# Kernel tuning notes

Hardware: AMD Instinct MI355X
Metric: run time of the kernel (lower is better)

Reference implementation:

```python
import jax, jax.numpy as jnp
import numpy as np

N_RAYS = 16384
PTS_PER_RAY = 256
M = N_RAYS * PTS_PER_RAY
ALPHA_INIT = 0.01


def setup_inputs() -> dict:
    key = jax.random.key(0)
    k1, k2 = jax.random.split(key)
    density = jax.random.normal(k1, (M,), dtype=jnp.float32)
    ray_id = jnp.sort(jax.random.randint(k2, (M,), 0, N_RAYS)).astype(jnp.int32)
    shift = jnp.full((1,), np.log(1.0 / (1.0 - ALPHA_INIT) - 1.0), dtype=jnp.float32)
    interval = jnp.full((1,), 0.5, dtype=jnp.float32)
    return {"density": density, "ray_id": ray_id, "shift": shift, "interval": interval, "N": N_RAYS}


def reference(density, ray_id, shift, interval, N):
    # Raw2Alpha: alpha = 1 - exp(-softplus(density + shift) * interval)
    #           => log(1 - alpha) = -softplus(density + shift) * interval (exact, stable)
    sp = jax.nn.softplus(density + shift[0])            # [M]
    log_one_minus_alpha = -sp * interval[0]             # [M], <= 0
    alpha = -jnp.expm1(log_one_minus_alpha)             # [M]

    # Alphas2Weights: per-ray exclusive cumprod of (1-alpha) in log space.
    cs = jnp.cumsum(log_one_minus_alpha)                # inclusive global cumsum
    ex = cs - log_one_minus_alpha                       # exclusive global cumsum (non-increasing)
    # value of ex at the first element of each ray = segment max (ex is non-increasing)
    base = jax.ops.segment_max(ex, ray_id, num_segments=N)  # [N]
    T = jnp.exp(ex - base[ray_id])                      # exclusive per-ray transmittance
    weights = T * alpha                                 # [M]
    # alphainv_last = prod(1-alpha) over each ray (empty rays -> 1)
    log_total = jax.ops.segment_sum(log_one_minus_alpha, ray_id, num_segments=N)
    alphainv_last = jnp.exp(log_total)                  # [N]
    return weights, alphainv_last
```

## Files before the change

kernel.cpp:

```cpp
#include <hip/hip_runtime.h>
#include <hip/hip_bf16.h>


#define EPL 8
#define CHUNK (64 * EPL)

__device__ __forceinline__ float wave_incl_scan(float x) {
    float v = x;
    v += __int_as_float(__builtin_amdgcn_update_dpp(0, __float_as_int(v), 0x111, 0xf, 0xf, true));
    v += __int_as_float(__builtin_amdgcn_update_dpp(0, __float_as_int(v), 0x112, 0xf, 0xf, true));
    v += __int_as_float(__builtin_amdgcn_update_dpp(0, __float_as_int(v), 0x114, 0xf, 0xf, true));
    v += __int_as_float(__builtin_amdgcn_update_dpp(0, __float_as_int(v), 0x118, 0xf, 0xf, true));
    v += __int_as_float(__builtin_amdgcn_update_dpp(0, __float_as_int(v), 0x142, 0xa, 0xf, false));
    v += __int_as_float(__builtin_amdgcn_update_dpp(0, __float_as_int(v), 0x143, 0xc, 0xf, false));
    return v;
}

__device__ __forceinline__ int lower_bound_gallop(const int* __restrict__ a,
                                                  int M, int key, int hint) {
    if (hint < 0) hint = 0;
    if (hint >= M) hint = M - 1;
    int lo, hi;
    if (a[hint] >= key) {
        int step = 32;
        hi = hint;
        lo = hint - step;
        while (lo >= 0 && a[lo] >= key) { hi = lo; step <<= 1; lo = hint - step; }
        if (lo < 0) lo = -1;
    } else {
        int step = 32;
        lo = hint;
        hi = hint + step;
        while (hi < M && a[hi] < key) { lo = hi; step <<= 1; hi = hint + step; }
        if (hi > M) hi = M;
    }
    while (hi - lo > 1) {
        const int mid = (lo + hi) >> 1;
        if (a[mid] >= key) hi = mid; else lo = mid;
    }
    return hi;
}

__global__ __launch_bounds__(256) void VoxelNeRF_fused(
    const float* __restrict__ density,
    const int*   __restrict__ ray_id,
    const float* __restrict__ shift_p,
    const float* __restrict__ interval_p,
    float* __restrict__ weights,
    float* __restrict__ alphainv_last,
    int M, int N) {
    const int wave = threadIdx.x >> 6;
    const int lane = threadIdx.x & 63;
    const int r = blockIdx.x * 4 + wave;
    if (r >= N) return;

    const int avg  = M / N;
    const int s = lower_bound_gallop(ray_id, M, r,     (int)(((long long)r * M) / N));
    const int e = lower_bound_gallop(ray_id, M, r + 1, s + avg);

    const float shift    = shift_p[0];
    const float interval = interval_p[0];

    float carry = 0.0f;
    const int a0 = s & ~(EPL - 1);

    for (int base = a0; base < e; base += CHUNK) {
        const int g = base + lane * EPL;

        float x8[EPL];
        if (g < e && g + EPL <= M) {
            const float4* p = reinterpret_cast<const float4*>(density + g);
            const float4 v0 = p[0];
            const float4 v1 = p[1];
            x8[0] = v0.x; x8[1] = v0.y; x8[2] = v0.z; x8[3] = v0.w;
            x8[4] = v1.x; x8[5] = v1.y; x8[6] = v1.z; x8[7] = v1.w;
        } else if (g < e) {
            #pragma unroll
            for (int k = 0; k < EPL; ++k) {
                const int i = g + k;
                x8[k] = (i < M) ? density[i] : 0.0f;
            }
        }

        float al[EPL], pk[EPL];
        float lane_sum = 0.0f;
        #pragma unroll
        for (int k = 0; k < EPL; ++k) {
            const int i = g + k;
            float lomk = 0.0f, alk = 0.0f;
            if (i >= s && i < e) {
                const float x  = x8[k] + shift;
                const float sp = fmaxf(x, 0.0f) + __logf(1.0f + __expf(-fabsf(x)));
                lomk = -sp * interval;
                alk  = 1.0f - __expf(lomk);
            }
            al[k] = alk;
            pk[k] = lane_sum;
            lane_sum += lomk;
        }

        const float v_incl  = wave_incl_scan(lane_sum);
        const float base_ex = carry + (v_incl - lane_sum);

        if (g >= s && g + EPL <= e) {
            float4 w0, w1;
            w0.x = __expf(base_ex + pk[0]) * al[0];
            w0.y = __expf(base_ex + pk[1]) * al[1];
            w0.z = __expf(base_ex + pk[2]) * al[2];
            w0.w = __expf(base_ex + pk[3]) * al[3];
            w1.x = __expf(base_ex + pk[4]) * al[4];
            w1.y = __expf(base_ex + pk[5]) * al[5];
            w1.z = __expf(base_ex + pk[6]) * al[6];
            w1.w = __expf(base_ex + pk[7]) * al[7];
            float4* q = reinterpret_cast<float4*>(weights + g);
            q[0] = w0;
            q[1] = w1;
        } else if (g + EPL > s && g < e) {
            #pragma unroll
            for (int k = 0; k < EPL; ++k) {
                const int i = g + k;
                if (i >= s && i < e) {
                    weights[i] = __expf(base_ex + pk[k]) * al[k];
                }
            }
        }

        carry += __int_as_float(__builtin_amdgcn_readlane(__float_as_int(v_incl), 63));
    }

    if (lane == 0) {
        alphainv_last[r] = __expf(carry);
    }
}

extern "C" void kernel_launch(void* const* d_in, const int* in_sizes, int n_in,
                              void* d_out, int out_size, void* d_ws, size_t ws_size,
                              hipStream_t stream) {
    const float* density    = (const float*)d_in[0];
    const int*   ray_id     = (const int*)d_in[1];
    const float* shift_p    = (const float*)d_in[2];
    const float* interval_p = (const float*)d_in[3];
    const int M = in_sizes[0];
    const int N = out_size - M;

    float* weights       = (float*)d_out;
    float* alphainv_last = (float*)d_out + M;

    const int waves_per_block = 4;
    const int blocks = (N + waves_per_block - 1) / waves_per_block;
    VoxelNeRF_fused<<<blocks, 256, 0, stream>>>(
        density, ray_id, shift_p, interval_p, weights, alphainv_last, M, N);
}
```

Measured before the change: 99.97 us.

## Precompute ray start offsets in a separate pass instead of per-wave galloping search

Adds a first kernel that reads ray_id in int4 chunks and writes a start-offset table into workspace, filling entries for empty rays as well. The scan kernel then reads each ray's bounds with two loads instead of running two galloping binary searches. This is meant to remove the long chain of dependent global loads at the start of every wave. In exchange it adds a full streaming read of ray_id, a workspace write and a second kernel launch.

```diff
diff --git a/kernel.cpp b/kernel.cpp
--- a/kernel.cpp
+++ b/kernel.cpp
@@ -16,34 +16,31 @@
     return v;
 }
 
-__device__ __forceinline__ int lower_bound_gallop(const int* __restrict__ a,
-                                                  int M, int key, int hint) {
-    if (hint < 0) hint = 0;
-    if (hint >= M) hint = M - 1;
-    int lo, hi;
-    if (a[hint] >= key) {
-        int step = 32;
-        hi = hint;
-        lo = hint - step;
-        while (lo >= 0 && a[lo] >= key) { hi = lo; step <<= 1; lo = hint - step; }
-        if (lo < 0) lo = -1;
-    } else {
-        int step = 32;
-        lo = hint;
-        hi = hint + step;
-        while (hi < M && a[hi] < key) { lo = hi; step <<= 1; hi = hint + step; }
-        if (hi > M) hi = M;
+__global__ void VoxelNeRF_find_starts(const int* __restrict__ ray_id,
+                                      int* __restrict__ start,
+                                      int M, int N) {
+    const int j  = blockIdx.x * blockDim.x + threadIdx.x;
+    const int i0 = j * 4;
+    if (i0 >= M) return;
+    const int4 v = *reinterpret_cast<const int4*>(ray_id + i0);
+    int prev = (i0 == 0) ? -1 : ray_id[i0 - 1];
+    const int ids0 = v.x, ids1 = v.y, ids2 = v.z, ids3 = v.w;
+    #pragma unroll
+    for (int k = 0; k < 4; ++k) {
+        const int cur = (k == 0) ? ids0 : (k == 1) ? ids1 : (k == 2) ? ids2 : ids3;
+        if (cur != prev) {
+            for (int r = prev + 1; r <= cur; ++r) start[r] = i0 + k;
+        }
+        prev = cur;
     }
-    while (hi - lo > 1) {
-        const int mid = (lo + hi) >> 1;
-        if (a[mid] >= key) hi = mid; else lo = mid;
+    if (i0 + 4 >= M) {
+        for (int r = prev + 1; r <= N; ++r) start[r] = M;
     }
-    return hi;
 }
 
-__global__ __launch_bounds__(256) void VoxelNeRF_fused(
+__global__ __launch_bounds__(256) void VoxelNeRF_scan(
     const float* __restrict__ density,
-    const int*   __restrict__ ray_id,
+    const int*   __restrict__ start,
     const float* __restrict__ shift_p,
     const float* __restrict__ interval_p,
     float* __restrict__ weights,
@@ -54,10 +51,8 @@
     const int r = blockIdx.x * 4 + wave;
     if (r >= N) return;
 
-    const int avg  = M / N;
-    const int s = lower_bound_gallop(ray_id, M, r,     (int)(((long long)r * M) / N));
-    const int e = lower_bound_gallop(ray_id, M, r + 1, s + avg);
-
+    const int s = start[r];
+    const int e = start[r + 1];
     const float shift    = shift_p[0];
     const float interval = interval_p[0];
 
@@ -145,9 +140,18 @@
 
     float* weights       = (float*)d_out;
     float* alphainv_last = (float*)d_out + M;
+    int*   start         = (int*)d_ws;
 
-    const int waves_per_block = 4;
-    const int blocks = (N + waves_per_block - 1) / waves_per_block;
-    VoxelNeRF_fused<<<blocks, 256, 0, stream>>>(
-        density, ray_id, shift_p, interval_p, weights, alphainv_last, M, N);
+    {
+        const int threads = 256;
+        const int elems   = (M + 3) / 4;
+        const int blocks  = (elems + threads - 1) / threads;
+        VoxelNeRF_find_starts<<<blocks, threads, 0, stream>>>(ray_id, start, M, N);
+    }
+    {
+        const int waves_per_block = 4;
+        const int blocks = (N + waves_per_block - 1) / waves_per_block;
+        VoxelNeRF_scan<<<blocks, 256, 0, stream>>>(
+            density, start, shift_p, interval_p, weights, alphainv_last, M, N);
+    }
 }
```

Measured after the change: 92.62 us. 1.08x faster.
